# Optimization experiments

Hardware: AMD Instinct MI355X
Metric: run time of the kernel (lower is better)

The kernel has to match this reference:

```python
import jax, jax.numpy as jnp
import numpy as np

NUM_EMBEDDINGS = 512
EMBEDDING_DIM = 100
COMMITMENT_COST = 0.25


def setup_inputs() -> dict:
    key = jax.random.key(0)
    k1, k2 = jax.random.split(key)
    inputs = jax.random.normal(k1, (64, 64, 64, EMBEDDING_DIM), dtype=jnp.float32)
    # nn.Embedding weight init: uniform(-1/num_embeddings, 1/num_embeddings)
    lim = 1.0 / NUM_EMBEDDINGS
    embedding = jax.random.uniform(k2, (NUM_EMBEDDINGS, EMBEDDING_DIM),
                                   dtype=jnp.float32, minval=-lim, maxval=lim)
    return {"inputs": inputs, "embedding": embedding}


def reference(inputs, embedding):
    d = inputs.shape[-1]
    flat = inputs.reshape(-1, d)                                  # [N, d]
    # squared L2 distances to each codebook entry: [N, K]
    distances = (jnp.sum(flat ** 2, axis=1, keepdims=True)
                 + jnp.sum(embedding ** 2, axis=1)
                 - 2.0 * flat @ embedding.T)
    encoding_indices = jnp.argmin(distances, axis=1)              # [N]
    quantized = embedding[encoding_indices].reshape(inputs.shape)
    commitment_loss = COMMITMENT_COST * jnp.mean(
        (jax.lax.stop_gradient(quantized) - inputs) ** 2)
    quantization_loss = jnp.mean(
        (quantized - jax.lax.stop_gradient(inputs)) ** 2)
    # straight-through estimator
    quantized_st = inputs + jax.lax.stop_gradient(quantized - inputs)
    return quantized_st, quantization_loss, commitment_loss
```

## Files before the change

### kernel.cpp

```cpp
#include <hip/hip_runtime.h>
#include <hip/hip_bf16.h>
#include <cfloat>


#define N_ROWS (64 * 64 * 64)
#define D 100
#define KCODES 512
#define CB_OFF 4096
#define E2_OFF 16

typedef __attribute__((ext_vector_type(8))) short short8;
typedef __attribute__((ext_vector_type(4))) float f32x4;

__device__ __forceinline__ unsigned short f2bf(float f) {
    union { float f; unsigned u; } v; v.f = f;
    unsigned r = v.u + 0x7FFF + ((v.u >> 16) & 1);
    return (unsigned short)(r >> 16);
}
__device__ __forceinline__ unsigned pk2(float a, float b) {
    union { __hip_bfloat162 h; unsigned u; } c;
    c.h = __float22bfloat162_rn(make_float2(a, b));
    return c.u;
}
__device__ __forceinline__ short8 pack8(const float4& a, const float4& b) {
    union { unsigned u[4]; short8 v; } r;
    r.u[0] = pk2(a.x, a.y); r.u[1] = pk2(a.z, a.w);
    r.u[2] = pk2(b.x, b.y); r.u[3] = pk2(b.z, b.w);
    return r.v;
}

__global__ __launch_bounds__(64) void vq_init(const float* __restrict__ emb,
                                              float* __restrict__ ws) {
    const int code = blockIdx.x, l = threadIdx.x;
    const float* e = emb + code * D;
    if (code == 0 && l == 0) ws[0] = 0.0f;
    float a = e[l];
    float b = (l < D - 64) ? e[64 + l] : 0.0f;
    float p = fmaf(a, a, b * b);
#pragma unroll
    for (int off = 32; off; off >>= 1) p += __shfl_xor(p, off);
    if (l == 0) ws[E2_OFF + code] = p;

    if (l < 16) {
        const int s = l >> 2, q = l & 3;
        short8 v;
#pragma unroll
        for (int j = 0; j < 8; ++j) {
            int k = s * 32 + q * 8 + j;
            v[j] = (k < D) ? (short)f2bf(e[k]) : (short)0;
        }
        const int chunk = code >> 5, ci = code & 31;
        const int tt = ci >> 4, lr = ci & 15;
        unsigned short* cb = (unsigned short*)((char*)ws + CB_OFF);
        *(short8*)(cb + chunk * 4096 + ((s * 2 + tt) * 64 + q * 16 + lr) * 8) = v;
    }
}

__global__ __launch_bounds__(256, 2) void vq_main(const float* __restrict__ x,
                                                  const float* __restrict__ emb,
                                                  float* __restrict__ ws,
                                                  float* __restrict__ out) {
    __shared__ uint4  bbuf[2][1024];
    __shared__ float  e2s[KCODES];
    __shared__ int    widx[256];
    __shared__ float  wsum[4];

    const int tid = threadIdx.x, wave = tid >> 6, lane = tid & 63;
    const int quad = lane >> 4, lr = lane & 15;
    const long brow = (long)blockIdx.x * 256;
    const long wrow = brow + wave * 64;

    float4 av[4][7];
#pragma unroll
    for (int m = 0; m < 4; ++m) {
        const float* xr = x + (wrow + m * 16 + lr) * D + quad * 8;
        av[m][0] = *(const float4*)(xr);
        av[m][1] = *(const float4*)(xr + 4);
        av[m][2] = *(const float4*)(xr + 32);
        av[m][3] = *(const float4*)(xr + 36);
        av[m][4] = *(const float4*)(xr + 64);
        av[m][5] = *(const float4*)(xr + 68);
        av[m][6] = *(const float4*)(x + (wrow + m * 16 + lr) * D + 96);
    }

    const uint4* __restrict__ cbg = (const uint4*)((const char*)ws + CB_OFF);
    uint4 st0 = cbg[wave * 128 + lane];
    uint4 st1 = cbg[wave * 128 + 64 + lane];
    uint4 st2 = cbg[512 + wave * 128 + lane];
    uint4 st3 = cbg[512 + wave * 128 + 64 + lane];
    const float* __restrict__ e2g = ws + E2_OFF;
    e2s[tid]       = e2g[tid];
    e2s[256 + tid] = e2g[256 + tid];

    short8 A[4][4];
    float  xnorm[4];
#pragma unroll
    for (int m = 0; m < 4; ++m) {
        float4 z = av[m][6];
        if (quad != 0) z = make_float4(0.f, 0.f, 0.f, 0.f);
        float nrm = 0.f;
#pragma unroll
        for (int i = 0; i < 6; ++i) {
            float4 f = av[m][i];
            nrm = fmaf(f.x, f.x, nrm); nrm = fmaf(f.y, f.y, nrm);
            nrm = fmaf(f.z, f.z, nrm); nrm = fmaf(f.w, f.w, nrm);
        }
        nrm = fmaf(z.x, z.x, nrm); nrm = fmaf(z.y, z.y, nrm);
        nrm = fmaf(z.z, z.z, nrm); nrm = fmaf(z.w, z.w, nrm);
        A[m][0] = pack8(av[m][0], av[m][1]);
        A[m][1] = pack8(av[m][2], av[m][3]);
        A[m][2] = pack8(av[m][4], av[m][5]);
        A[m][3] = pack8(z, make_float4(0.f, 0.f, 0.f, 0.f));
        nrm += __shfl_xor(nrm, 16);
        nrm += __shfl_xor(nrm, 32);
        xnorm[m] = nrm;
    }

    bbuf[0][wave * 128 + lane]             = st0;
    bbuf[0][wave * 128 + 64 + lane]        = st1;
    bbuf[0][512 + wave * 128 + lane]       = st2;
    bbuf[0][512 + wave * 128 + 64 + lane]  = st3;
    __syncthreads();

    float    runmin[4][4];
    unsigned runidx[4][4];
#pragma unroll
    for (int m = 0; m < 4; ++m)
#pragma unroll
        for (int r = 0; r < 4; ++r) { runmin[m][r] = FLT_MAX; runidx[m][r] = 0; }

#pragma unroll 1
    for (int j = 0; j < 8; ++j) {
        const int p = j & 1;
        uint4 n0, n1, n2, n3;
        if (j < 7) {
            n0 = cbg[(j + 1) * 1024 + wave * 128 + lane];
            n1 = cbg[(j + 1) * 1024 + wave * 128 + 64 + lane];
            n2 = cbg[(j + 1) * 1024 + 512 + wave * 128 + lane];
            n3 = cbg[(j + 1) * 1024 + 512 + wave * 128 + 64 + lane];
        }

#pragma unroll
        for (int cc = 0; cc < 2; ++cc) {
            const int c = j * 2 + cc;
            const short8* __restrict__ bl = (const short8*)&bbuf[p][cc * 512];
            short8 B[2][4];
#pragma unroll
            for (int s = 0; s < 4; ++s) {
                B[0][s] = bl[(s * 2 + 0) * 64 + lane];
                B[1][s] = bl[(s * 2 + 1) * 64 + lane];
            }
            float e2v0 = e2s[c * 32 + lr];
            float e2v1 = e2s[c * 32 + 16 + lr];

            f32x4 acc[4][2];
#pragma unroll
            for (int m = 0; m < 4; ++m) {
                acc[m][0] = (f32x4){0.f, 0.f, 0.f, 0.f};
                acc[m][1] = (f32x4){0.f, 0.f, 0.f, 0.f};
            }
#pragma unroll
            for (int s = 0; s < 4; ++s)
#pragma unroll
                for (int m = 0; m < 4; ++m) {
                    acc[m][0] = __builtin_amdgcn_mfma_f32_16x16x32_bf16(A[m][s], B[0][s], acc[m][0], 0, 0, 0);
                    acc[m][1] = __builtin_amdgcn_mfma_f32_16x16x32_bf16(A[m][s], B[1][s], acc[m][1], 0, 0, 0);
                }

#pragma unroll
            for (int m = 0; m < 4; ++m)
#pragma unroll
                for (int tt = 0; tt < 2; ++tt) {
                    float e2v = tt ? e2v1 : e2v0;
                    unsigned code = c * 32 + tt * 16 + lr;
#pragma unroll
                    for (int r = 0; r < 4; ++r) {
                        float sc = fmaf(-2.0f, acc[m][tt][r], e2v);
                        if (sc < runmin[m][r]) { runmin[m][r] = sc; runidx[m][r] = code; }
                    }
                }
        }

        if (j < 7) {
            bbuf[p ^ 1][wave * 128 + lane]            = n0;
            bbuf[p ^ 1][wave * 128 + 64 + lane]       = n1;
            bbuf[p ^ 1][512 + wave * 128 + lane]      = n2;
            bbuf[p ^ 1][512 + wave * 128 + 64 + lane] = n3;
        }
        __syncthreads();
    }

    float lsum = 0.0f;
#pragma unroll
    for (int m = 0; m < 4; ++m)
#pragma unroll
        for (int r = 0; r < 4; ++r) {
            float    s = runmin[m][r];
            unsigned i = runidx[m][r];
#pragma unroll
            for (int off = 8; off >= 1; off >>= 1) {
                float    os = __shfl_xor(s, off);
                unsigned oi = (unsigned)__shfl_xor((int)i, off);
                if (os < s || (os == s && oi < i)) { s = os; i = oi; }
            }
            if (lr == quad * 4 + r) {
                lsum += xnorm[m] + s;
                widx[wave * 64 + m * 16 + quad * 4 + r] = (int)i;
            }
        }
#pragma unroll
    for (int off = 32; off >= 1; off >>= 1) lsum += __shfl_xor(lsum, off);
    if (lane == 0) wsum[wave] = lsum;
    __syncthreads();
    if (tid == 0) atomicAdd(ws, wsum[0] + wsum[1] + wsum[2] + wsum[3]);

    const float4* __restrict__ ef = (const float4*)emb;
    float4* __restrict__ og = (float4*)(out + brow * D);
#pragma unroll
    for (int i = 0; i < 25; i += 5) {
        float4 q[5];
        int    gi[5];
#pragma unroll
        for (int u = 0; u < 5; ++u) {
            int g = (i + u) * 256 + tid;
            int row = g / 25;
            int c4  = g - row * 25;
            gi[u] = g;
            q[u]  = ef[(long)widx[row] * 25 + c4];
        }
#pragma unroll
        for (int u = 0; u < 5; ++u) og[gi[u]] = q[u];
    }
}

__global__ void vq_final(const float* __restrict__ ws, float* __restrict__ out) {
    float mse = ws[0] / (float)((long)N_ROWS * D);
    out[(long)N_ROWS * D]     = mse;
    out[(long)N_ROWS * D + 1] = 0.25f * mse;
}

extern "C" void kernel_launch(void* const* d_in, const int* in_sizes, int n_in,
                              void* d_out, int out_size, void* d_ws, size_t ws_size,
                              hipStream_t stream) {
    const float* x   = (const float*)d_in[0];
    const float* emb = (const float*)d_in[1];
    float* out = (float*)d_out;
    float* ws  = (float*)d_ws;

    vq_init<<<KCODES, 64, 0, stream>>>(emb, ws);
    vq_main<<<N_ROWS / 256, 256, 0, stream>>>(x, emb, ws, out);
    vq_final<<<1, 1, 0, stream>>>(ws, out);
}
```

Measured before the change: 226.9 us.

## Fold codebook norm into MFMA and pack argmin index into float mantissa

Each codebook entry's -0.5·||e||² is stored as an extra bf16 element in its padded K slot, and the input row gets a matching 1.0, so the MFMA directly yields x·e - 0.5||e||². The shared-memory e2 table and the per-element FMA go away. The running argmin becomes a single fmaxf over floats whose low 9 mantissa bits carry a reversed code index, which removes the compare-and-select of a separate index register. In exchange it truncates score precision, rounds the norm bias to bf16, and changes tie-breaking behaviour for negative scores.

After: 214.6 us (median of 2 runs). -5.4%, faster.

```diff
diff --git a/kernel.cpp b/kernel.cpp
--- a/kernel.cpp
+++ b/kernel.cpp
@@ -27,6 +27,12 @@
     r.u[0] = pk2(a.x, a.y); r.u[1] = pk2(a.z, a.w);
     r.u[2] = pk2(b.x, b.y); r.u[3] = pk2(b.z, b.w);
     return r.v;
+}
+__device__ __forceinline__ unsigned f2u(float f) {
+    union { float f; unsigned u; } v; v.f = f; return v.u;
+}
+__device__ __forceinline__ float u2f(unsigned u) {
+    union { unsigned u; float f; } v; v.u = u; return v.f;
 }
 
 __global__ __launch_bounds__(64) void vq_init(const float* __restrict__ emb,
@@ -49,6 +55,7 @@
             int k = s * 32 + q * 8 + j;
             v[j] = (k < D) ? (short)f2bf(e[k]) : (short)0;
         }
+        if (l == 12) v[4] = (short)f2bf(-0.5f * p);
         const int chunk = code >> 5, ci = code & 31;
         const int tt = ci >> 4, lr = ci & 15;
         unsigned short* cb = (unsigned short*)((char*)ws + CB_OFF);
@@ -61,12 +68,12 @@
                                                   float* __restrict__ ws,
                                                   float* __restrict__ out) {
     __shared__ uint4  bbuf[2][1024];
-    __shared__ float  e2s[KCODES];
     __shared__ int    widx[256];
     __shared__ float  wsum[4];
 
     const int tid = threadIdx.x, wave = tid >> 6, lane = tid & 63;
     const int quad = lane >> 4, lr = lane & 15;
+    const int lrc = 15 - lr;
     const long brow = (long)blockIdx.x * 256;
     const long wrow = brow + wave * 64;
 
@@ -88,12 +95,10 @@
     uint4 st1 = cbg[wave * 128 + 64 + lane];
     uint4 st2 = cbg[512 + wave * 128 + lane];
     uint4 st3 = cbg[512 + wave * 128 + 64 + lane];
-    const float* __restrict__ e2g = ws + E2_OFF;
-    e2s[tid]       = e2g[tid];
-    e2s[256 + tid] = e2g[256 + tid];
 
     short8 A[4][4];
     float  xnorm[4];
+    const float4 one0 = make_float4(quad == 0 ? 1.f : 0.f, 0.f, 0.f, 0.f);
 #pragma unroll
     for (int m = 0; m < 4; ++m) {
         float4 z = av[m][6];
@@ -110,7 +115,7 @@
         A[m][0] = pack8(av[m][0], av[m][1]);
         A[m][1] = pack8(av[m][2], av[m][3]);
         A[m][2] = pack8(av[m][4], av[m][5]);
-        A[m][3] = pack8(z, make_float4(0.f, 0.f, 0.f, 0.f));
+        A[m][3] = pack8(z, one0);
         nrm += __shfl_xor(nrm, 16);
         nrm += __shfl_xor(nrm, 32);
         xnorm[m] = nrm;
@@ -122,12 +127,11 @@
     bbuf[0][512 + wave * 128 + 64 + lane]  = st3;
     __syncthreads();
 
-    float    runmin[4][4];
-    unsigned runidx[4][4];
+    float runpk[4][4];
 #pragma unroll
     for (int m = 0; m < 4; ++m)
 #pragma unroll
-        for (int r = 0; r < 4; ++r) { runmin[m][r] = FLT_MAX; runidx[m][r] = 0; }
+        for (int r = 0; r < 4; ++r) runpk[m][r] = -FLT_MAX;
 
 #pragma unroll 1
     for (int j = 0; j < 8; ++j) {
@@ -150,8 +154,6 @@
                 B[0][s] = bl[(s * 2 + 0) * 64 + lane];
                 B[1][s] = bl[(s * 2 + 1) * 64 + lane];
             }
-            float e2v0 = e2s[c * 32 + lr];
-            float e2v1 = e2s[c * 32 + 16 + lr];
 
             f32x4 acc[4][2];
 #pragma unroll
@@ -167,17 +169,15 @@
                     acc[m][1] = __builtin_amdgcn_mfma_f32_16x16x32_bf16(A[m][s], B[1][s], acc[m][1], 0, 0, 0);
                 }
 
+            const int ib0 = (31 - (c * 2 + 0)) * 16 + lrc;
+            const int ib1 = (31 - (c * 2 + 1)) * 16 + lrc;
 #pragma unroll
             for (int m = 0; m < 4; ++m)
 #pragma unroll
-                for (int tt = 0; tt < 2; ++tt) {
-                    float e2v = tt ? e2v1 : e2v0;
-                    unsigned code = c * 32 + tt * 16 + lr;
-#pragma unroll
-                    for (int r = 0; r < 4; ++r) {
-                        float sc = fmaf(-2.0f, acc[m][tt][r], e2v);
-                        if (sc < runmin[m][r]) { runmin[m][r] = sc; runidx[m][r] = code; }
-                    }
+                for (int r = 0; r < 4; ++r) {
+                    float p0 = u2f((f2u(acc[m][0][r]) & ~511u) | (unsigned)ib0);
+                    float p1 = u2f((f2u(acc[m][1][r]) & ~511u) | (unsigned)ib1);
+                    runpk[m][r] = fmaxf(runpk[m][r], fmaxf(p0, p1));
                 }
         }
 
@@ -195,17 +195,15 @@
     for (int m = 0; m < 4; ++m)
 #pragma unroll
         for (int r = 0; r < 4; ++r) {
-            float    s = runmin[m][r];
-            unsigned i = runidx[m][r];
-#pragma unroll
-            for (int off = 8; off >= 1; off >>= 1) {
-                float    os = __shfl_xor(s, off);
-                unsigned oi = (unsigned)__shfl_xor((int)i, off);
-                if (os < s || (os == s && oi < i)) { s = os; i = oi; }
-            }
+            float s = runpk[m][r];
+#pragma unroll
+            for (int off = 8; off >= 1; off >>= 1)
+                s = fmaxf(s, __shfl_xor(s, off));
             if (lr == quad * 4 + r) {
-                lsum += xnorm[m] + s;
-                widx[wave * 64 + m * 16 + quad * 4 + r] = (int)i;
+                unsigned u = f2u(s);
+                int code = 511 - (int)(u & 511u);
+                lsum += fmaf(-2.0f, s, xnorm[m]);
+                widx[wave * 64 + m * 16 + quad * 4 + r] = code;
             }
         }
 #pragma unroll
```
